# Kernel tuning notes

Measured on AMD Instinct MI355X. Metric: run time of the kernel, lower is better.

Reference implementation:

```python
import jax, jax.numpy as jnp
import numpy as np

B, T, C = 4, 2048, 768
H, D = 12, 64          # num_heads, head_size
R = 64                 # kv_lora_rank
ROPE_THETA = 10000.0


def setup_inputs() -> dict:
    key = jax.random.key(0)
    ks = jax.random.split(key, 8)
    s = lambda fan_in: 1.0 / np.sqrt(fan_in)
    return {
        "x":      jax.random.normal(ks[0], (B, T, C), jnp.float32),
        "Wq":     jax.random.normal(ks[1], (C, H * D), jnp.float32) * s(C),
        "Wdown":  jax.random.normal(ks[2], (C, R), jnp.float32) * s(C),
        "ln_g":   jnp.ones((R,), jnp.float32),
        "ln_b":   jnp.zeros((R,), jnp.float32),
        "Wup":    jax.random.normal(ks[3], (R, 2 * H * D), jnp.float32) * s(R),
        "Wo":     jax.random.normal(ks[4], (H * D, C), jnp.float32) * s(H * D),
        "bo":     jnp.zeros((C,), jnp.float32),
    }


def _rope_cos_sin(t, d, dtype):
    # freqs over half-dim, repeated twice (rotate-half convention)
    inv_freq = 1.0 / (ROPE_THETA ** (jnp.arange(0, d, 2, dtype=jnp.float32) / d))
    ang = jnp.arange(t, dtype=jnp.float32)[:, None] * inv_freq[None, :]  # [T, D/2]
    ang = jnp.concatenate([ang, ang], axis=-1)                            # [T, D]
    return jnp.cos(ang).astype(dtype), jnp.sin(ang).astype(dtype)


def _apply_rope(q, cos, sin):
    # q: [B, H, T, D]; cos/sin: [T, D]
    d2 = q.shape[-1] // 2
    rot = jnp.concatenate([-q[..., d2:], q[..., :d2]], axis=-1)
    return q * cos + rot * sin


def reference(x, Wq, Wdown, ln_g, ln_b, Wup, Wo, bo):
    b, t, c = x.shape
    q = (x @ Wq).reshape(b, t, H, D).transpose(0, 2, 1, 3)  # [B,H,T,D]

    ckv = x @ Wdown                                         # [B,T,R]
    mu = jnp.mean(ckv, axis=-1, keepdims=True)
    var = jnp.var(ckv, axis=-1, keepdims=True)
    ckv = (ckv - mu) * jax.lax.rsqrt(var + 1e-5) * ln_g + ln_b

    kv = (ckv @ Wup).reshape(b, t, 2, H, D)
    k = kv[:, :, 0].transpose(0, 2, 1, 3)                   # [B,H,T,D]
    v = kv[:, :, 1].transpose(0, 2, 1, 3)

    cos, sin = _rope_cos_sin(t, D, x.dtype)
    q = _apply_rope(q, cos, sin)
    k = _apply_rope(k, cos, sin)

    wei = jnp.einsum("bhqd,bhkd->bhqk", q, k) * (D ** -0.5)
    causal = jnp.tril(jnp.ones((t, t), bool))
    wei = jnp.where(causal, wei, -jnp.inf)
    wei = jax.nn.softmax(wei, axis=-1)                      # dropout: eval mode (identity)

    out = jnp.einsum("bhqk,bhkd->bhqd", wei, v)             # [B,H,T,D]
    out = out.transpose(0, 2, 1, 3).reshape(b, t, H * D)
    return out @ Wo + bo
```

## Files before the change

### kernel.cpp

```cpp
#include <hip/hip_runtime.h>
#include <hip/hip_bf16.h>
#include <math.h>

#define B_ 4
#define T_ 2048
#define C_ 768
#define H_ 12
#define D_ 64
#define R_ 64
#define BT_ (B_*T_)
#define HD_ (H_*D_)

typedef __attribute__((ext_vector_type(8))) short bf16x8;
typedef __attribute__((ext_vector_type(4))) float f32x4;
typedef __attribute__((ext_vector_type(16))) float f32x16;

__device__ inline short f2bf(float f) {
  union { float f; unsigned u; } x; x.f = f;
  unsigned r = x.u + 0x7fffu + ((x.u >> 16) & 1u);
  return (short)(r >> 16);
}
__device__ inline unsigned pk_bf16(float a, float b) {
#if __has_builtin(__builtin_amdgcn_cvt_pk_bf16_f32)
  auto t = __builtin_amdgcn_cvt_pk_bf16_f32(a, b);
  unsigned u; __builtin_memcpy(&u, &t, sizeof(unsigned)); return u;
#else
  union { float f; unsigned u; } x, y; x.f = a; y.f = b;
  unsigned ra = (x.u + 0x7fffu + ((x.u >> 16) & 1u)) >> 16;
  unsigned rb = (y.u + 0x7fffu + ((y.u >> 16) & 1u)) & 0xffff0000u;
  return ra | rb;
#endif
}
__device__ inline float fexp2(float x) {
#if __has_builtin(__builtin_amdgcn_exp2f)
  return __builtin_amdgcn_exp2f(x);
#else
  return exp2f(x);
#endif
}
__device__ inline void pswap(unsigned &a, unsigned &b) {
#if __has_builtin(__builtin_amdgcn_permlane32_swap)
  auto r = __builtin_amdgcn_permlane32_swap((int)a, (int)b, false, false);
  unsigned u[2]; __builtin_memcpy(u, &r, 8);
  a = u[0]; b = u[1];
#else
  unsigned ax = __shfl_xor(a, 32), bx = __shfl_xor(b, 32);
  bool hi = (threadIdx.x & 32) != 0;
  unsigned na = hi ? bx : a;
  unsigned nb = hi ? b : ax;
  a = na; b = nb;
#endif
}
typedef __attribute__((address_space(3))) unsigned lds_u32;
typedef __attribute__((address_space(1))) const unsigned glb_u32;
__device__ inline void gload_lds16(const void* g, void* l) {
  __builtin_amdgcn_global_load_lds((glb_u32*)g, (lds_u32*)l, 16, 0, 0);
}

__device__ inline void ttile(const float* __restrict__ src, short* __restrict__ dst,
                             int K, int N, int k0, int n0, int tid, float (*tl)[33]) {
  int tx = tid & 31, ty = tid >> 5;
  #pragma unroll
  for (int r = 0; r < 4; ++r)
    tl[ty + 8 * r][tx] = src[(size_t)(k0 + ty + 8 * r) * N + n0 + tx];
  __syncthreads();
  #pragma unroll
  for (int r = 0; r < 4; ++r)
    dst[(size_t)(n0 + ty + 8 * r) * K + k0 + tx] = f2bf(tl[tx][ty + 8 * r]);
}

__global__ __launch_bounds__(256) void prep_conv(
    const float* __restrict__ Wq, const float* __restrict__ Wd,
    const float* __restrict__ Wup, const float* __restrict__ Wo,
    short* __restrict__ W1T, short* __restrict__ WupT, short* __restrict__ WoT,
    float* __restrict__ cs, float* __restrict__ sn) {
  __shared__ float tl[32][33];
  int tid = threadIdx.x;
  int blk = blockIdx.x;
  if (blk < 576) {
    int tk = blk % 24, tn = blk / 24;
    ttile(Wq, W1T, 768, 768, tk * 32, tn * 32, tid, tl);
  } else if (blk < 624) {
    int l = blk - 576; int tk = l % 24, tn = l / 24;
    ttile(Wd, W1T + (size_t)768 * 768, 768, 64, tk * 32, tn * 32, tid, tl);
  } else if (blk < 720) {
    int l = blk - 624; int tk = l % 2, tn = l / 2;
    ttile(Wup, WupT, 64, 1536, tk * 32, tn * 32, tid, tl);
  } else if (blk < 1296) {
    int l = blk - 720; int tk = l % 24, tn = l / 24;
    ttile(Wo, WoT, 768, 768, tk * 32, tn * 32, tid, tl);
  } else {
    int base = (blk - 1296) * 1024;
    #pragma unroll
    for (int i = 0; i < 4; ++i) {
      int idx = base + tid + i * 256;
      int j = idx & 31, t = idx >> 5;
      float invf = exp2f(-(float)j * (13.287712379549449f / 32.f));
      float a = (float)t * invf;
      cs[idx] = cosf(a);
      sn[idx] = sinf(a);
    }
  }
}

#define SC2_ 0.18033688f

template<int MODE>
__global__ __launch_bounds__(256) void gemm128(
    const float* __restrict__ Af, const short* __restrict__ Ab,
    const short* __restrict__ Bt,
    int M, int N, int K,
    const float* __restrict__ bias, const float* __restrict__ bias2,
    short* __restrict__ ob0, short* __restrict__ ob1,
    const float* __restrict__ cs, const float* __restrict__ sn)
{
  constexpr int NBUF = (MODE == 0) ? 2 : 1;
  __shared__ short SM[NBUF * 2 * 128 * 64];
  const int m0 = blockIdx.x * 128;
  const int n0 = blockIdx.y * 128;
  const int tid = threadIdx.x, lane = tid & 63, w = tid >> 6;
  const int wr = w >> 1, wc = w & 1;
  const int fr = lane & 15, fk = (lane >> 4) * 8;
  const int rstage = lane >> 3;
  const int cstage = (lane & 7) * 8;

  f32x4 acc[4][4] = {};

  auto As = [&](int buf) -> short* { return SM + buf * 16384; };
  auto Bs = [&](int buf) -> short* { return SM + buf * 16384 + 8192; };

  auto compute = [&](const short* Asb, const short* Bsb) {
    #pragma unroll
    for (int kk = 0; kk < 64; kk += 32) {
      bf16x8 a[4], b[4];
      #pragma unroll
      for (int mi = 0; mi < 4; ++mi)
        a[mi] = *(const bf16x8*)&Asb[(wr * 64 + mi * 16 + fr) * 64 + kk + fk];
      #pragma unroll
      for (int ni = 0; ni < 4; ++ni)
        b[ni] = *(const bf16x8*)&Bsb[(wc * 64 + ni * 16 + fr) * 64 + kk + fk];
      #pragma unroll
      for (int mi = 0; mi < 4; ++mi)
        #pragma unroll
        for (int ni = 0; ni < 4; ++ni)
          acc[mi][ni] = __builtin_amdgcn_mfma_f32_16x16x32_bf16(a[mi], b[ni], acc[mi][ni], 0, 0, 0);
    }
  };

  auto stageB = [&](short* Bsb, int k0) {
    #pragma unroll
    for (int i = 0; i < 4; ++i) {
      int c = w * 4 + i;
      int r = c * 8 + rstage;
      gload_lds16(&Bt[(size_t)(n0 + r) * K + k0 + cstage], Bsb + c * 512);
    }
  };

  if constexpr (MODE == 0) {
    float4 fa[8];
    auto loadA = [&](int k0) {
      #pragma unroll
      for (int i = 0; i < 4; ++i) {
        int idx = tid + 256 * i;
        int row = idx >> 3, c8 = idx & 7;
        const float* src = Af + (size_t)(m0 + row) * 768 + k0 + c8 * 8;
        fa[2 * i]     = *(const float4*)(src);
        fa[2 * i + 1] = *(const float4*)(src + 4);
      }
    };
    auto writeA = [&](short* Asb) {
      #pragma unroll
      for (int i = 0; i < 4; ++i) {
        int idx = tid + 256 * i;
        int row = idx >> 3, c8 = idx & 7;
        uint4 uu;
        uu.x = pk_bf16(fa[2 * i].x,     fa[2 * i].y);
        uu.y = pk_bf16(fa[2 * i].z,     fa[2 * i].w);
        uu.z = pk_bf16(fa[2 * i + 1].x, fa[2 * i + 1].y);
        uu.w = pk_bf16(fa[2 * i + 1].z, fa[2 * i + 1].w);
        *(uint4*)&Asb[row * 64 + c8 * 8] = uu;
      }
    };

    loadA(0);
    stageB(Bs(0), 0);
    writeA(As(0));
    __syncthreads();

    int buf = 0;
    for (int k0 = 0; k0 < K; k0 += 64) {
      bool nxt = (k0 + 64 < K);
      if (nxt) { loadA(k0 + 64); stageB(Bs(buf ^ 1), k0 + 64); }
      compute(As(buf), Bs(buf));
      if (nxt) writeA(As(buf ^ 1));
      __syncthreads();
      buf ^= 1;
    }
  } else {
    #pragma unroll
    for (int i = 0; i < 4; ++i) {
      int c = w * 4 + i;
      int r = c * 8 + rstage;
      gload_lds16(&Ab[(size_t)(m0 + r) * K + cstage], As(0) + c * 512);
      gload_lds16(&Bt[(size_t)(n0 + r) * K + cstage], Bs(0) + c * 512);
    }
    __syncthreads();
    compute(As(0), Bs(0));
  }

  const int er = (lane >> 4) * 4, ec = lane & 15;
  const int cb = n0 + wc * 64;

  if (cb < 768) {
    int h = cb >> 6;
    #pragma unroll
    for (int mi = 0; mi < 4; ++mi)
      #pragma unroll
      for (int r = 0; r < 4; ++r) {
        int row = m0 + wr * 64 + mi * 16 + er + r;
        int t = row & (T_ - 1), bb = row >> 11;
        short* dst = ob0 + (((size_t)(bb * H_ + h)) * T_ + t) * 64;
        #pragma unroll
        for (int ni = 0; ni < 2; ++ni) {
          int d = ni * 16 + ec;
          float c = cs[t * 32 + d], s = sn[t * 32 + d];
          if constexpr (MODE == 0) { c *= SC2_; s *= SC2_; }
          float x0 = acc[mi][ni][r], x1 = acc[mi][ni + 2][r];
          dst[d]      = f2bf(x0 * c - x1 * s);
          dst[d + 32] = f2bf(x1 * c + x0 * s);
        }
      }
  } else if constexpr (MODE == 0) {
    if (cb == 768) {
      #pragma unroll
      for (int mi = 0; mi < 4; ++mi)
        #pragma unroll
        for (int r = 0; r < 4; ++r) {
          float s = 0.f, s2 = 0.f;
          #pragma unroll
          for (int ni = 0; ni < 4; ++ni) { float v = acc[mi][ni][r]; s += v; s2 += v*v; }
          #pragma unroll
          for (int off = 1; off < 16; off <<= 1) {
            s  += __shfl_xor(s, off);
            s2 += __shfl_xor(s2, off);
          }
          float mu = s * (1.f/64.f);
          float var = s2 * (1.f/64.f) - mu * mu;
          float rstd = rsqrtf(var + 1e-5f);
          int row = m0 + wr * 64 + mi * 16 + er + r;
          #pragma unroll
          for (int ni = 0; ni < 4; ++ni) {
            int d = ni * 16 + ec;
            ob1[(size_t)row * 64 + d] = f2bf((acc[mi][ni][r] - mu) * rstd * bias[d] + bias2[d]);
          }
        }
    }
  } else {
    __syncthreads();
    short* Wl = SM + w * 2560;
    int h = (cb - 768) >> 6;
    int bb = m0 >> 11;
    int dl = lane >> 2, tl = (lane & 3) * 8;
    #pragma unroll
    for (int hp = 0; hp < 2; ++hp) {
      #pragma unroll
      for (int mi2 = 0; mi2 < 2; ++mi2) {
        int mi = hp * 2 + mi2;
        int tl0 = mi2 * 16 + er;
        #pragma unroll
        for (int ni = 0; ni < 4; ++ni) {
          int d = ni * 16 + ec;
          uint2 uu;
          uu.x = pk_bf16(acc[mi][ni][0], acc[mi][ni][1]);
          uu.y = pk_bf16(acc[mi][ni][2], acc[mi][ni][3]);
          *(uint2*)&Wl[d * 40 + tl0] = uu;
        }
      }
      int tg0 = (m0 & (T_ - 1)) + wr * 64 + hp * 32;
      #pragma unroll
      for (int j = 0; j < 4; ++j) {
        int d = j * 16 + dl;
        uint4 vv = *(const uint4*)&Wl[d * 40 + tl];
        *(uint4*)&ob1[((size_t)(bb * H_ + h) * 64 + d) * T_ + tg0 + tl] = vv;
      }
    }
  }
}

__global__ __launch_bounds__(256) void gemm_out(
    const short* __restrict__ A, const short* __restrict__ Bt,
    int M, int N, int K,
    float* __restrict__ out0, const float* __restrict__ bias)
{
  __shared__ short SM[2 * (128 * 64 + 64 * 64)];
  const int m0 = blockIdx.x * 128;
  const int n0 = blockIdx.y * 64;
  const int tid = threadIdx.x, lane = tid & 63, w = tid >> 6;
  const int fr = lane & 15, fk = (lane >> 4) * 8;
  const int rstage = lane >> 3;
  const int cstage = (lane & 7) * 8;

  f32x4 acc[2][4] = {};

  auto As = [&](int buf) -> short* { return SM + buf * 12288; };
  auto Bs = [&](int buf) -> short* { return SM + buf * 12288 + 8192; };

  auto stage = [&](int buf, int k0) {
    #pragma unroll
    for (int i = 0; i < 4; ++i) {
      int c = w * 4 + i;
      int r = c * 8 + rstage;
      gload_lds16(&A[(size_t)(m0 + r) * K + k0 + cstage], As(buf) + c * 512);
    }
    #pragma unroll
    for (int i = 0; i < 2; ++i) {
      int c = w * 2 + i;
      int r = c * 8 + rstage;
      gload_lds16(&Bt[(size_t)(n0 + r) * K + k0 + cstage], Bs(buf) + c * 512);
    }
  };

  stage(0, 0);
  __syncthreads();

  int buf = 0;
  for (int k0 = 0; k0 < K; k0 += 64) {
    if (k0 + 64 < K) stage(buf ^ 1, k0 + 64);
    #pragma unroll
    for (int kk = 0; kk < 64; kk += 32) {
      bf16x8 a[2], b[4];
      a[0] = *(const bf16x8*)&As(buf)[(w * 32 +      fr) * 64 + kk + fk];
      a[1] = *(const bf16x8*)&As(buf)[(w * 32 + 16 + fr) * 64 + kk + fk];
      #pragma unroll
      for (int ni = 0; ni < 4; ++ni)
        b[ni] = *(const bf16x8*)&Bs(buf)[(ni * 16 + fr) * 64 + kk + fk];
      #pragma unroll
      for (int mi = 0; mi < 2; ++mi)
        #pragma unroll
        for (int ni = 0; ni < 4; ++ni)
          acc[mi][ni] = __builtin_amdgcn_mfma_f32_16x16x32_bf16(a[mi], b[ni], acc[mi][ni], 0, 0, 0);
    }
    __syncthreads();
    buf ^= 1;
  }

  const int er = (lane >> 4) * 4, ec = lane & 15;
  #pragma unroll
  for (int mi = 0; mi < 2; ++mi)
    #pragma unroll
    for (int r = 0; r < 4; ++r) {
      int row = m0 + w * 32 + mi * 16 + er + r;
      #pragma unroll
      for (int ni = 0; ni < 4; ++ni) {
        int col = n0 + ni * 16 + ec;
        out0[(size_t)row * N + col] = acc[mi][ni][r] + bias[col];
      }
    }
}

__global__ __launch_bounds__(256) void attn_mfma(
    const short* __restrict__ qgl, const short* __restrict__ kg,
    const short* __restrict__ vtg, short* __restrict__ o)
{
  __shared__ short SMa[2][2][8 * 512];

  const int bh = blockIdx.x;
  const int u  = 15 - blockIdx.y;
  const int tid = threadIdx.x, lane = tid & 63, w = tid >> 6;
  const int q32 = lane & 31, half = lane >> 5;
  const short* kb  = kg  + (size_t)bh * T_ * 64;
  const short* vtb = vtg + (size_t)bh * 64 * T_;
  const int b = bh / H_, h = bh - b * H_;

  const int wq = 4 * u + w;
  const int q0 = wq * 32;
  const int last_w = (wq >> 1) * 64;
  const int qidx = q0 + q32;
  const int kend = (2 * u + 1) * 64;

  const short* qrow = qgl + ((size_t)bh * T_ + qidx) * 64;
  bf16x8 bq[4];
  #pragma unroll
  for (int ks = 0; ks < 4; ++ks)
    bq[ks] = *(const bf16x8*)&qrow[ks * 16 + half * 8];

  f32x16 oacc[2] = {};
  float lrun = 0.f;

  auto stage = [&](int buf, int kt) {
    #pragma unroll
    for (int i = 0; i < 2; ++i) {
      int c = w * 2 + i;
      int kh = c >> 2, ks = c & 3;
      gload_lds16(kb + (size_t)(kt + kh * 32 + q32) * 64 + ks * 16 + half * 8,
                  &SMa[buf][0][c * 512]);
      gload_lds16(vtb + (size_t)(kh * 32 + q32) * T_ + kt + ks * 16 + half * 8,
                  &SMa[buf][1][c * 512]);
    }
  };

  stage(0, 0);
  __syncthreads();

  int cur = 0;
  for (int kt = 0; kt <= kend; kt += 64) {
    if (kt + 64 <= kend) stage(cur ^ 1, kt + 64);

    if (kt <= last_w) {
      const short* Kc = &SMa[cur][0][0];
      const short* Vc = &SMa[cur][1][0];
      const bool diag = (kt == last_w);
      const int dkh = diag ? (wq & 1) : 2;
      const bool skip1 = diag && ((wq & 1) == 0);

      bf16x8 bp[4];
      #pragma unroll
      for (int kh = 0; kh < 2; ++kh) {
        if (kh == 1 && skip1) break;
        f32x16 sacc = {};
        __builtin_amdgcn_s_setprio(1);
        #pragma unroll
        for (int ks = 0; ks < 4; ++ks) {
          bf16x8 a = *(const bf16x8*)&Kc[(kh * 4 + ks) * 512 + lane * 8];
          sacc = __builtin_amdgcn_mfma_f32_32x32x16_bf16(a, bq[ks], sacc, 0, 0, 0);
        }
        __builtin_amdgcn_s_setprio(0);
        float pv[16];
        if (kh != dkh) {
          #pragma unroll
          for (int r = 0; r < 16; ++r) pv[r] = fexp2(sacc[r]);
        } else {
          #pragma unroll
          for (int r = 0; r < 16; ++r) {
            int key = kt + kh * 32 + (r & 3) + 8 * (r >> 2) + 4 * half;
            pv[r] = (key <= qidx) ? fexp2(sacc[r]) : 0.f;
          }
        }
        float t0 = (pv[0] + pv[1]) + (pv[2] + pv[3]);
        float t1 = (pv[4] + pv[5]) + (pv[6] + pv[7]);
        float t2 = (pv[8] + pv[9]) + (pv[10] + pv[11]);
        float t3 = (pv[12] + pv[13]) + (pv[14] + pv[15]);
        lrun += (t0 + t1) + (t2 + t3);
        unsigned l0 = pk_bf16(pv[0],  pv[1]),  h0 = pk_bf16(pv[2],  pv[3]);
        unsigned l1 = pk_bf16(pv[4],  pv[5]),  h1 = pk_bf16(pv[6],  pv[7]);
        unsigned l2 = pk_bf16(pv[8],  pv[9]),  h2 = pk_bf16(pv[10], pv[11]);
        unsigned l3 = pk_bf16(pv[12], pv[13]), h3 = pk_bf16(pv[14], pv[15]);
        pswap(l0, l1); pswap(h0, h1);
        pswap(l2, l3); pswap(h2, h3);
        union { unsigned u[4]; bf16x8 v; } f0, f1;
        f0.u[0] = l0; f0.u[1] = h0; f0.u[2] = l1; f0.u[3] = h1;
        f1.u[0] = l2; f1.u[1] = h2; f1.u[2] = l3; f1.u[3] = h3;
        bp[2 * kh + 0] = f0.v;
        bp[2 * kh + 1] = f1.v;
      }

      __builtin_amdgcn_s_setprio(1);
      #pragma unroll
      for (int ks = 0; ks < 2; ++ks)
        #pragma unroll
        for (int dt = 0; dt < 2; ++dt) {
          bf16x8 av = *(const bf16x8*)&Vc[(dt * 4 + ks) * 512 + lane * 8];
          oacc[dt] = __builtin_amdgcn_mfma_f32_32x32x16_bf16(av, bp[ks], oacc[dt], 0, 0, 0);
        }
      if (!skip1) {
        #pragma unroll
        for (int ks = 2; ks < 4; ++ks)
          #pragma unroll
          for (int dt = 0; dt < 2; ++dt) {
            bf16x8 av = *(const bf16x8*)&Vc[(dt * 4 + ks) * 512 + lane * 8];
            oacc[dt] = __builtin_amdgcn_mfma_f32_32x32x16_bf16(av, bp[ks], oacc[dt], 0, 0, 0);
          }
      }
      __builtin_amdgcn_s_setprio(0);
    }

    __syncthreads();
    cur ^= 1;
  }

  float ltot = lrun + __shfl_xor(lrun, 32);
  float inv = 1.f / ltot;
  short* Pw = &SMa[0][0][0] + w * 2304;
  #pragma unroll
  for (int dt = 0; dt < 2; ++dt)
    #pragma unroll
    for (int g2 = 0; g2 < 4; ++g2) {
      uint2 uu;
      uu.x = pk_bf16(oacc[dt][4 * g2 + 0] * inv, oacc[dt][4 * g2 + 1] * inv);
      uu.y = pk_bf16(oacc[dt][4 * g2 + 2] * inv, oacc[dt][4 * g2 + 3] * inv);
      *(uint2*)&Pw[q32 * 72 + dt * 32 + 8 * g2 + 4 * half] = uu;
    }
  int row = lane >> 1, seg = lane & 1;
  int t = q0 + row;
  short* orow = o + ((size_t)(b * T_ + t)) * HD_ + h * 64 + seg * 32;
  #pragma unroll
  for (int i = 0; i < 4; ++i) {
    uint4 vv = *(const uint4*)&Pw[row * 72 + seg * 32 + i * 8];
    *(uint4*)&orow[i * 8] = vv;
  }
}

extern "C" void kernel_launch(void* const* d_in, const int* in_sizes, int n_in,
                              void* d_out, int out_size, void* d_ws, size_t ws_size,
                              hipStream_t stream) {
  (void)in_sizes; (void)n_in; (void)out_size; (void)ws_size;
  const float* x     = (const float*)d_in[0];
  const float* Wq    = (const float*)d_in[1];
  const float* Wdown = (const float*)d_in[2];
  const float* ln_g  = (const float*)d_in[3];
  const float* ln_b  = (const float*)d_in[4];
  const float* Wup   = (const float*)d_in[5];
  const float* Wo    = (const float*)d_in[6];
  const float* bo    = (const float*)d_in[7];
  float* out = (float*)d_out;

  char* w = (char*)d_ws;
  short* W1T    = (short*)w;  w += (size_t)896 * C_    * 2;
  short* WupT   = (short*)w;  w += (size_t)2*HD_ * R_  * 2;
  short* WoT    = (short*)w;  w += (size_t)HD_ * C_    * 2;
  short* ckv    = (short*)w;  w += (size_t)BT_ * R_    * 2;
  short* qb     = (short*)w;  w += (size_t)BT_ * HD_   * 2;
  short* kb     = (short*)w;  w += (size_t)BT_ * HD_   * 2;
  short* vt     = (short*)w;  w += (size_t)BT_ * HD_   * 2;
  short* att    = (short*)w;  w += (size_t)BT_ * HD_   * 2;
  float* cs_t   = (float*)w;  w += (size_t)T_ * 32 * 4;
  float* sn_t   = (float*)w;  w += (size_t)T_ * 32 * 4;

  prep_conv<<<1360, 256, 0, stream>>>(Wq, Wdown, Wup, Wo,
                                      W1T, WupT, WoT, cs_t, sn_t);

  gemm128<0><<<dim3(BT_/128, 7), 256, 0, stream>>>(
      x, nullptr, W1T, BT_, 832, C_, ln_g, ln_b, qb, ckv, cs_t, sn_t);

  gemm128<1><<<dim3(BT_/128, 12), 256, 0, stream>>>(
      nullptr, ckv, WupT, BT_, 2*HD_, R_, nullptr, nullptr, kb, vt, cs_t, sn_t);

  attn_mfma<<<dim3(B_*H_, 16), 256, 0, stream>>>(qb, kb, vt, att);

  gemm_out<<<dim3(BT_/128, 12), 256, 0, stream>>>(
      att, WoT, BT_, C_, HD_, out, bo);
}
```

Before: 194.4 us.

## Fuse all stages into one persistent cooperative kernel with grid syncs

Turns the five separate kernels into device bodies and runs them inside a single cooperative persistent kernel of 512 blocks, with grid.sync between stages. Attention tiles are handed out through an atomic work counter so blocks pick up the heavy causal tiles first. The aim is to remove launch gaps and tail idle time between stages. In exchange, every stage now uses a fixed 64KB shared allocation at two blocks per CU, which can lower occupancy and add grid-barrier cost. If the cooperative launch fails, it falls back to the separate kernels.

```diff
diff --git a/kernel.cpp b/kernel.cpp
--- a/kernel.cpp
+++ b/kernel.cpp
@@ -1,5 +1,6 @@
 #include <hip/hip_runtime.h>
 #include <hip/hip_bf16.h>
+#include <hip/hip_cooperative_groups.h>
 #include <math.h>
 
 #define B_ 4
@@ -57,8 +58,12 @@
   __builtin_amdgcn_global_load_lds((glb_u32*)g, (lds_u32*)l, 16, 0, 0);
 }
 
-__device__ inline void ttile(const float* __restrict__ src, short* __restrict__ dst,
-                             int K, int N, int k0, int n0, int tid, float (*tl)[33]) {
+#define SC2_ 0.18033688f
+
+
+__device__ __attribute__((always_inline)) inline void ttile(
+    const float* __restrict__ src, short* __restrict__ dst,
+    int K, int N, int k0, int n0, int tid, float (*tl)[33]) {
   int tx = tid & 31, ty = tid >> 5;
   #pragma unroll
   for (int r = 0; r < 4; ++r)
@@ -69,14 +74,11 @@
     dst[(size_t)(n0 + ty + 8 * r) * K + k0 + tx] = f2bf(tl[tx][ty + 8 * r]);
 }
 
-__global__ __launch_bounds__(256) void prep_conv(
-    const float* __restrict__ Wq, const float* __restrict__ Wd,
-    const float* __restrict__ Wup, const float* __restrict__ Wo,
-    short* __restrict__ W1T, short* __restrict__ WupT, short* __restrict__ WoT,
-    float* __restrict__ cs, float* __restrict__ sn) {
-  __shared__ float tl[32][33];
-  int tid = threadIdx.x;
-  int blk = blockIdx.x;
+__device__ __attribute__((always_inline)) inline void prep_unit(
+    int blk, int tid, char* smemc,
+    const float* Wq, const float* Wd, const float* Wup, const float* Wo,
+    short* W1T, short* WupT, short* WoT, float* cs, float* sn) {
+  float (*tl)[33] = (float(*)[33])smemc;
   if (blk < 576) {
     int tk = blk % 24, tn = blk / 24;
     ttile(Wq, W1T, 768, 768, tk * 32, tn * 32, tid, tl);
@@ -103,21 +105,16 @@
   }
 }
 
-#define SC2_ 0.18033688f
-
 template<int MODE>
-__global__ __launch_bounds__(256) void gemm128(
+__device__ __attribute__((always_inline)) inline void gemm128_body(
+    int m0, int n0, char* smemc,
     const float* __restrict__ Af, const short* __restrict__ Ab,
-    const short* __restrict__ Bt,
-    int M, int N, int K,
+    const short* __restrict__ Bt, int K,
     const float* __restrict__ bias, const float* __restrict__ bias2,
     short* __restrict__ ob0, short* __restrict__ ob1,
     const float* __restrict__ cs, const float* __restrict__ sn)
 {
-  constexpr int NBUF = (MODE == 0) ? 2 : 1;
-  __shared__ short SM[NBUF * 2 * 128 * 64];
-  const int m0 = blockIdx.x * 128;
-  const int n0 = blockIdx.y * 128;
+  short* SM = (short*)smemc;
   const int tid = threadIdx.x, lane = tid & 63, w = tid >> 6;
   const int wr = w >> 1, wc = w & 1;
   const int fr = lane & 15, fk = (lane >> 4) * 8;
@@ -287,14 +284,13 @@
   }
 }
 
-__global__ __launch_bounds__(256) void gemm_out(
+__device__ __attribute__((always_inline)) inline void gemmout_body(
+    int m0, int n0, char* smemc,
     const short* __restrict__ A, const short* __restrict__ Bt,
-    int M, int N, int K,
     float* __restrict__ out0, const float* __restrict__ bias)
 {
-  __shared__ short SM[2 * (128 * 64 + 64 * 64)];
-  const int m0 = blockIdx.x * 128;
-  const int n0 = blockIdx.y * 64;
+  short* SM = (short*)smemc;
+  const int K = HD_, N = C_;
   const int tid = threadIdx.x, lane = tid & 63, w = tid >> 6;
   const int fr = lane & 15, fk = (lane >> 4) * 8;
   const int rstage = lane >> 3;
@@ -358,14 +354,14 @@
     }
 }
 
-__global__ __launch_bounds__(256) void attn_mfma(
+__device__ __attribute__((always_inline)) inline void attn_body(
+    int bh, int u, char* smemc,
     const short* __restrict__ qgl, const short* __restrict__ kg,
     const short* __restrict__ vtg, short* __restrict__ o)
 {
-  __shared__ short SMa[2][2][8 * 512];
-
-  const int bh = blockIdx.x;
-  const int u  = 15 - blockIdx.y;
+  typedef short KVBUF[2][8 * 512];
+  KVBUF* SMa = (KVBUF*)smemc;
+
   const int tid = threadIdx.x, lane = tid & 63, w = tid >> 6;
   const int q32 = lane & 31, half = lane >> 5;
   const short* kb  = kg  + (size_t)bh * T_ * 64;
@@ -480,7 +476,7 @@
 
   float ltot = lrun + __shfl_xor(lrun, 32);
   float inv = 1.f / ltot;
-  short* Pw = &SMa[0][0][0] + w * 2304;
+  short* Pw = (short*)smemc + w * 2304;
   #pragma unroll
   for (int dt = 0; dt < 2; ++dt)
     #pragma unroll
@@ -498,6 +494,94 @@
     uint4 vv = *(const uint4*)&Pw[row * 72 + seg * 32 + i * 8];
     *(uint4*)&orow[i * 8] = vv;
   }
+}
+
+struct MegaArgs {
+  const float *x, *Wq, *Wd, *ln_g, *ln_b, *Wup, *Wo, *bo;
+  float *out;
+  short *W1T, *WupT, *WoT, *ckv, *qb, *kb, *vt, *att;
+  float *cs, *sn;
+  unsigned *qcnt;
+};
+
+namespace cg = cooperative_groups;
+
+__global__ __launch_bounds__(256, 2) void mega(MegaArgs A) {
+  __shared__ __align__(16) char SMEM[65536];
+  const int blk = blockIdx.x;
+  const int tid = threadIdx.x;
+  cg::grid_group grid = cg::this_grid();
+
+  if (blk == 0 && tid == 0) *A.qcnt = 0u;
+
+  for (int p = blk; p < 1360; p += 512) {
+    prep_unit(p, tid, SMEM, A.Wq, A.Wd, A.Wup, A.Wo, A.W1T, A.WupT, A.WoT, A.cs, A.sn);
+    __syncthreads();
+  }
+  grid.sync();
+
+  if (blk < 448) {
+    int bx = blk & 63, by = blk >> 6;
+    gemm128_body<0>(bx * 128, by * 128, SMEM, A.x, nullptr, A.W1T, 768,
+                    A.ln_g, A.ln_b, A.qb, A.ckv, A.cs, A.sn);
+  }
+  grid.sync();
+
+  for (int p = blk; p < 768; p += 512) {
+    int bx = p & 63, by = p >> 6;
+    gemm128_body<1>(bx * 128, by * 128, SMEM, nullptr, A.ckv, A.WupT, 64,
+                    nullptr, nullptr, A.kb, A.vt, A.cs, A.sn);
+    __syncthreads();
+  }
+  grid.sync();
+
+  unsigned* qslot = (unsigned*)(SMEM + 65532);
+  for (;;) {
+    __syncthreads();
+    if (tid == 0) *qslot = atomicAdd(A.qcnt, 1u);
+    __syncthreads();
+    unsigned q = *qslot;
+    if (q >= 768u) break;
+    attn_body((int)(q % 48u), 15 - (int)(q / 48u), SMEM, A.qb, A.kb, A.vt, A.att);
+  }
+  grid.sync();
+
+  for (int p = blk; p < 768; p += 512) {
+    int bx = p & 63, by = p >> 6;
+    gemmout_body(bx * 128, by * 64, SMEM, A.att, A.WoT, A.out, A.bo);
+    __syncthreads();
+  }
+}
+
+__global__ __launch_bounds__(256) void prep_conv_k(
+    const float* Wq, const float* Wd, const float* Wup, const float* Wo,
+    short* W1T, short* WupT, short* WoT, float* cs, float* sn) {
+  __shared__ __align__(16) char s[4352];
+  prep_unit(blockIdx.x, threadIdx.x, s, Wq, Wd, Wup, Wo, W1T, WupT, WoT, cs, sn);
+}
+__global__ __launch_bounds__(256) void gemm0_k(
+    const float* x, const short* W1T, const float* ln_g, const float* ln_b,
+    short* qb, short* ckv, const float* cs, const float* sn) {
+  __shared__ __align__(16) char s[65536];
+  gemm128_body<0>(blockIdx.x * 128, blockIdx.y * 128, s, x, nullptr, W1T, 768,
+                  ln_g, ln_b, qb, ckv, cs, sn);
+}
+__global__ __launch_bounds__(256) void gemm1_k(
+    const short* ckv, const short* WupT, short* kb, short* vt,
+    const float* cs, const float* sn) {
+  __shared__ __align__(16) char s[32768];
+  gemm128_body<1>(blockIdx.x * 128, blockIdx.y * 128, s, nullptr, ckv, WupT, 64,
+                  nullptr, nullptr, kb, vt, cs, sn);
+}
+__global__ __launch_bounds__(256) void attn_k(
+    const short* qb, const short* kb, const short* vt, short* att) {
+  __shared__ __align__(16) char s[32768];
+  attn_body(blockIdx.x, 15 - (int)blockIdx.y, s, qb, kb, vt, att);
+}
+__global__ __launch_bounds__(256) void gemmout_k(
+    const short* att, const short* WoT, float* out, const float* bo) {
+  __shared__ __align__(16) char s[49152];
+  gemmout_body(blockIdx.x * 128, blockIdx.y * 64, s, att, WoT, out, bo);
 }
 
 extern "C" void kernel_launch(void* const* d_in, const int* in_sizes, int n_in,
@@ -525,18 +609,23 @@
   short* att    = (short*)w;  w += (size_t)BT_ * HD_   * 2;
   float* cs_t   = (float*)w;  w += (size_t)T_ * 32 * 4;
   float* sn_t   = (float*)w;  w += (size_t)T_ * 32 * 4;
-
-  prep_conv<<<1360, 256, 0, stream>>>(Wq, Wdown, Wup, Wo,
-                                      W1T, WupT, WoT, cs_t, sn_t);
-
-  gemm128<0><<<dim3(BT_/128, 7), 256, 0, stream>>>(
-      x, nullptr, W1T, BT_, 832, C_, ln_g, ln_b, qb, ckv, cs_t, sn_t);
-
-  gemm128<1><<<dim3(BT_/128, 12), 256, 0, stream>>>(
-      nullptr, ckv, WupT, BT_, 2*HD_, R_, nullptr, nullptr, kb, vt, cs_t, sn_t);
-
-  attn_mfma<<<dim3(B_*H_, 16), 256, 0, stream>>>(qb, kb, vt, att);
-
-  gemm_out<<<dim3(BT_/128, 12), 256, 0, stream>>>(
-      att, WoT, BT_, C_, HD_, out, bo);
-}
+  unsigned* qcnt = (unsigned*)w; w += 64;
+
+  MegaArgs ma;
+  ma.x = x; ma.Wq = Wq; ma.Wd = Wdown; ma.ln_g = ln_g; ma.ln_b = ln_b;
+  ma.Wup = Wup; ma.Wo = Wo; ma.bo = bo; ma.out = out;
+  ma.W1T = W1T; ma.WupT = WupT; ma.WoT = WoT; ma.ckv = ckv;
+  ma.qb = qb; ma.kb = kb; ma.vt = vt; ma.att = att;
+  ma.cs = cs_t; ma.sn = sn_t; ma.qcnt = qcnt;
+  void* kargs[] = { &ma };
+
+  hipError_t e = hipLaunchCooperativeKernel((const void*)mega, dim3(512), dim3(256),
+                                            kargs, 0, stream);
+  if (e != hipSuccess) {
+    prep_conv_k<<<1360, 256, 0, stream>>>(Wq, Wdown, Wup, Wo, W1T, WupT, WoT, cs_t, sn_t);
+    gemm0_k<<<dim3(64, 7), 256, 0, stream>>>(x, W1T, ln_g, ln_b, qb, ckv, cs_t, sn_t);
+    gemm1_k<<<dim3(64, 12), 256, 0, stream>>>(ckv, WupT, kb, vt, cs_t, sn_t);
+    attn_k<<<dim3(48, 16), 256, 0, stream>>>(qb, kb, vt, att);
+    gemmout_k<<<dim3(64, 12), 256, 0, stream>>>(att, WoT, out, bo);
+  }
+}
```

Measured after the change: 474.5 us. +144.0%, slower.

## Absorb V up-projection into output weights and attend over shared latent

Applied to the files above, without the earlier changes.

Precomputes per-head products of the V half of Wup with Wo in the prep kernel. Attention then consumes the transposed normalized latent (shared across heads) instead of per-head V. gemm0 writes the latent in transposed layout, and the KV up-projection now only computes K. This removes the V half of the up-projection GEMM and its per-head V writes and reads, at the cost of a small fp32 weight-product in prep and extra bf16 rounding of the fused weight.

```diff
diff --git a/kernel.cpp b/kernel.cpp
--- a/kernel.cpp
+++ b/kernel.cpp
@@ -57,75 +57,96 @@
   __builtin_amdgcn_global_load_lds((glb_u32*)g, (lds_u32*)l, 16, 0, 0);
 }
 
-__device__ inline void ttile(const float* __restrict__ src, short* __restrict__ dst,
-                             int K, int N, int k0, int n0, int tid, float (*tl)[33]) {
+#define SC2_ 0.18033688f
+
+__device__ __attribute__((always_inline)) inline void ttile(
+    const float* __restrict__ src, short* __restrict__ dst,
+    int Kd, int Ns, int k0, int n0, int tid, float (*tl)[33]) {
   int tx = tid & 31, ty = tid >> 5;
   #pragma unroll
   for (int r = 0; r < 4; ++r)
-    tl[ty + 8 * r][tx] = src[(size_t)(k0 + ty + 8 * r) * N + n0 + tx];
+    tl[ty + 8 * r][tx] = src[(size_t)(k0 + ty + 8 * r) * Ns + n0 + tx];
   __syncthreads();
   #pragma unroll
   for (int r = 0; r < 4; ++r)
-    dst[(size_t)(n0 + ty + 8 * r) * K + k0 + tx] = f2bf(tl[tx][ty + 8 * r]);
+    dst[(size_t)(n0 + ty + 8 * r) * Kd + k0 + tx] = f2bf(tl[tx][ty + 8 * r]);
 }
 
 __global__ __launch_bounds__(256) void prep_conv(
     const float* __restrict__ Wq, const float* __restrict__ Wd,
     const float* __restrict__ Wup, const float* __restrict__ Wo,
-    short* __restrict__ W1T, short* __restrict__ WupT, short* __restrict__ WoT,
+    short* __restrict__ W1T, short* __restrict__ WupT, short* __restrict__ WvoT,
     float* __restrict__ cs, float* __restrict__ sn) {
-  __shared__ float tl[32][33];
-  int tid = threadIdx.x;
-  int blk = blockIdx.x;
+  __shared__ float SH[32 * 65 + 64 * 33];
+  float (*tl)[33] = (float(*)[33])SH;
+  int tid = threadIdx.x, blk = blockIdx.x;
   if (blk < 576) {
     int tk = blk % 24, tn = blk / 24;
     ttile(Wq, W1T, 768, 768, tk * 32, tn * 32, tid, tl);
   } else if (blk < 624) {
     int l = blk - 576; int tk = l % 24, tn = l / 24;
     ttile(Wd, W1T + (size_t)768 * 768, 768, 64, tk * 32, tn * 32, tid, tl);
-  } else if (blk < 720) {
+  } else if (blk < 672) {
     int l = blk - 624; int tk = l % 2, tn = l / 2;
     ttile(Wup, WupT, 64, 1536, tk * 32, tn * 32, tid, tl);
-  } else if (blk < 1296) {
-    int l = blk - 720; int tk = l % 24, tn = l / 24;
-    ttile(Wo, WoT, 768, 768, tk * 32, tn * 32, tid, tl);
+  } else if (blk < 1248) {
+    int l = blk - 672;
+    int h = l / 48, rem = l % 48, tc = rem >> 1, tr = rem & 1;
+    float* a  = SH;
+    float* bm = SH + 32 * 65;
+    #pragma unroll
+    for (int i = 0; i < 8; ++i) {
+      int idx = tid + i * 256;
+      int r = idx >> 6, d = idx & 63;
+      a[r * 65 + d] = Wup[(size_t)(tr * 32 + r) * 1536 + 768 + h * 64 + d];
+      int dd = idx >> 5, c = idx & 31;
+      bm[dd * 33 + c] = Wo[(size_t)(h * 64 + dd) * 768 + tc * 32 + c];
+    }
+    __syncthreads();
+    int r = tid & 31, cj = tid >> 5;
+    float s0 = 0.f, s1 = 0.f, s2 = 0.f, s3 = 0.f;
+    #pragma unroll
+    for (int d = 0; d < 64; ++d) {
+      float av = a[r * 65 + d];
+      const float* bp = &bm[d * 33 + cj * 4];
+      s0 += av * bp[0]; s1 += av * bp[1]; s2 += av * bp[2]; s3 += av * bp[3];
+    }
+    int colb = tc * 32 + cj * 4;
+    size_t krow = (size_t)(h * 64 + tr * 32 + r);
+    WvoT[(size_t)(colb + 0) * 768 + krow] = f2bf(s0);
+    WvoT[(size_t)(colb + 1) * 768 + krow] = f2bf(s1);
+    WvoT[(size_t)(colb + 2) * 768 + krow] = f2bf(s2);
+    WvoT[(size_t)(colb + 3) * 768 + krow] = f2bf(s3);
   } else {
-    int base = (blk - 1296) * 1024;
+    int base = (blk - 1248) * 1024;
     #pragma unroll
     for (int i = 0; i < 4; ++i) {
       int idx = base + tid + i * 256;
       int j = idx & 31, t = idx >> 5;
       float invf = exp2f(-(float)j * (13.287712379549449f / 32.f));
-      float a = (float)t * invf;
-      cs[idx] = cosf(a);
-      sn[idx] = sinf(a);
-    }
-  }
-}
-
-#define SC2_ 0.18033688f
-
-template<int MODE>
-__global__ __launch_bounds__(256) void gemm128(
-    const float* __restrict__ Af, const short* __restrict__ Ab,
-    const short* __restrict__ Bt,
-    int M, int N, int K,
+      float ang = (float)t * invf;
+      cs[idx] = cosf(ang);
+      sn[idx] = sinf(ang);
+    }
+  }
+}
+
+__global__ __launch_bounds__(256) void gemm0_k(
+    const float* __restrict__ Af, const short* __restrict__ Bt,
     const float* __restrict__ bias, const float* __restrict__ bias2,
-    short* __restrict__ ob0, short* __restrict__ ob1,
+    short* __restrict__ ob0, short* __restrict__ ob1, short* __restrict__ obT,
     const float* __restrict__ cs, const float* __restrict__ sn)
 {
-  constexpr int NBUF = (MODE == 0) ? 2 : 1;
-  __shared__ short SM[NBUF * 2 * 128 * 64];
+  constexpr int K = 768;
+  __shared__ short SM[2 * 16384];
   const int m0 = blockIdx.x * 128;
   const int n0 = blockIdx.y * 128;
   const int tid = threadIdx.x, lane = tid & 63, w = tid >> 6;
   const int wr = w >> 1, wc = w & 1;
   const int fr = lane & 15, fk = (lane >> 4) * 8;
-  const int rstage = lane >> 3;
-  const int cstage = (lane & 7) * 8;
+  const int rstage = lane >> 3, cstage = (lane & 7) * 8;
 
   f32x4 acc[4][4] = {};
-
   auto As = [&](int buf) -> short* { return SM + buf * 16384; };
   auto Bs = [&](int buf) -> short* { return SM + buf * 16384 + 8192; };
 
@@ -146,7 +167,6 @@
           acc[mi][ni] = __builtin_amdgcn_mfma_f32_16x16x32_bf16(a[mi], b[ni], acc[mi][ni], 0, 0, 0);
     }
   };
-
   auto stageB = [&](short* Bsb, int k0) {
     #pragma unroll
     for (int i = 0; i < 4; ++i) {
@@ -156,56 +176,44 @@
     }
   };
 
-  if constexpr (MODE == 0) {
-    float4 fa[8];
-    auto loadA = [&](int k0) {
-      #pragma unroll
-      for (int i = 0; i < 4; ++i) {
-        int idx = tid + 256 * i;
-        int row = idx >> 3, c8 = idx & 7;
-        const float* src = Af + (size_t)(m0 + row) * 768 + k0 + c8 * 8;
-        fa[2 * i]     = *(const float4*)(src);
-        fa[2 * i + 1] = *(const float4*)(src + 4);
-      }
-    };
-    auto writeA = [&](short* Asb) {
-      #pragma unroll
-      for (int i = 0; i < 4; ++i) {
-        int idx = tid + 256 * i;
-        int row = idx >> 3, c8 = idx & 7;
-        uint4 uu;
-        uu.x = pk_bf16(fa[2 * i].x,     fa[2 * i].y);
-        uu.y = pk_bf16(fa[2 * i].z,     fa[2 * i].w);
-        uu.z = pk_bf16(fa[2 * i + 1].x, fa[2 * i + 1].y);
-        uu.w = pk_bf16(fa[2 * i + 1].z, fa[2 * i + 1].w);
-        *(uint4*)&Asb[row * 64 + c8 * 8] = uu;
-      }
-    };
-
-    loadA(0);
-    stageB(Bs(0), 0);
-    writeA(As(0));
+  float4 fa[8];
+  auto loadA = [&](int k0) {
+    #pragma unroll
+    for (int i = 0; i < 4; ++i) {
+      int idx = tid + 256 * i;
+      int row = idx >> 3, c8 = idx & 7;
+      const float* src = Af + (size_t)(m0 + row) * 768 + k0 + c8 * 8;
+      fa[2 * i]     = *(const float4*)(src);
+      fa[2 * i + 1] = *(const float4*)(src + 4);
+    }
+  };
+  auto writeA = [&](short* Asb) {
+    #pragma unroll
+    for (int i = 0; i < 4; ++i) {
+      int idx = tid + 256 * i;
+      int row = idx >> 3, c8 = idx & 7;
+      uint4 uu;
+      uu.x = pk_bf16(fa[2 * i].x,     fa[2 * i].y);
+      uu.y = pk_bf16(fa[2 * i].z,     fa[2 * i].w);
+      uu.z = pk_bf16(fa[2 * i + 1].x, fa[2 * i + 1].y);
+      uu.w = pk_bf16(fa[2 * i + 1].z, fa[2 * i + 1].w);
+      *(uint4*)&Asb[row * 64 + c8 * 8] = uu;
+    }
+  };
+
+  loadA(0);
+  stageB(Bs(0), 0);
+  writeA(As(0));
+  __syncthreads();
+
+  int buf = 0;
+  for (int k0 = 0; k0 < K; k0 += 64) {
+    bool nxt = (k0 + 64 < K);
+    if (nxt) { loadA(k0 + 64); stageB(Bs(buf ^ 1), k0 + 64); }
+    compute(As(buf), Bs(buf));
+    if (nxt) writeA(As(buf ^ 1));
     __syncthreads();
-
-    int buf = 0;
-    for (int k0 = 0; k0 < K; k0 += 64) {
-      bool nxt = (k0 + 64 < K);
-      if (nxt) { loadA(k0 + 64); stageB(Bs(buf ^ 1), k0 + 64); }
-      compute(As(buf), Bs(buf));
-      if (nxt) writeA(As(buf ^ 1));
-      __syncthreads();
-      buf ^= 1;
-    }
-  } else {
-    #pragma unroll
-    for (int i = 0; i < 4; ++i) {
-      int c = w * 4 + i;
-      int r = c * 8 + rstage;
-      gload_lds16(&Ab[(size_t)(m0 + r) * K + cstage], As(0) + c * 512);
-      gload_lds16(&Bt[(size_t)(n0 + r) * K + cstage], Bs(0) + c * 512);
-    }
-    __syncthreads();
-    compute(As(0), Bs(0));
+    buf ^= 1;
   }
 
   const int er = (lane >> 4) * 4, ec = lane & 15;
@@ -223,56 +231,51 @@
         #pragma unroll
         for (int ni = 0; ni < 2; ++ni) {
           int d = ni * 16 + ec;
-          float c = cs[t * 32 + d], s = sn[t * 32 + d];
-          if constexpr (MODE == 0) { c *= SC2_; s *= SC2_; }
+          float c = cs[t * 32 + d] * SC2_, s = sn[t * 32 + d] * SC2_;
           float x0 = acc[mi][ni][r], x1 = acc[mi][ni + 2][r];
           dst[d]      = f2bf(x0 * c - x1 * s);
           dst[d + 32] = f2bf(x1 * c + x0 * s);
         }
       }
-  } else if constexpr (MODE == 0) {
-    if (cb == 768) {
-      #pragma unroll
-      for (int mi = 0; mi < 4; ++mi)
+  } else if (cb == 768) {
+    short* Wl = SM + w * 2560;
+    int bb = m0 >> 11;
+    int dl = lane >> 2, tlo = (lane & 3) * 8;
+    #pragma unroll
+    for (int hp = 0; hp < 2; ++hp) {
+      #pragma unroll
+      for (int mi2 = 0; mi2 < 2; ++mi2) {
+        int mi = hp * 2 + mi2;
+        short vb[4][4];
         #pragma unroll
         for (int r = 0; r < 4; ++r) {
           float s = 0.f, s2 = 0.f;
           #pragma unroll
-          for (int ni = 0; ni < 4; ++ni) { float v = acc[mi][ni][r]; s += v; s2 += v*v; }
+          for (int ni = 0; ni < 4; ++ni) { float v = acc[mi][ni][r]; s += v; s2 += v * v; }
           #pragma unroll
           for (int off = 1; off < 16; off <<= 1) {
             s  += __shfl_xor(s, off);
             s2 += __shfl_xor(s2, off);
           }
-          float mu = s * (1.f/64.f);
-          float var = s2 * (1.f/64.f) - mu * mu;
+          float mu = s * (1.f / 64.f);
+          float var = s2 * (1.f / 64.f) - mu * mu;
           float rstd = rsqrtf(var + 1e-5f);
           int row = m0 + wr * 64 + mi * 16 + er + r;
           #pragma unroll
           for (int ni = 0; ni < 4; ++ni) {
             int d = ni * 16 + ec;
-            ob1[(size_t)row * 64 + d] = f2bf((acc[mi][ni][r] - mu) * rstd * bias[d] + bias2[d]);
+            short q = f2bf((acc[mi][ni][r] - mu) * rstd * bias[d] + bias2[d]);
+            vb[r][ni] = q;
+            ob1[(size_t)row * 64 + d] = q;
           }
         }
-    }
-  } else {
-    __syncthreads();
-    short* Wl = SM + w * 2560;
-    int h = (cb - 768) >> 6;
-    int bb = m0 >> 11;
-    int dl = lane >> 2, tl = (lane & 3) * 8;
-    #pragma unroll
-    for (int hp = 0; hp < 2; ++hp) {
-      #pragma unroll
-      for (int mi2 = 0; mi2 < 2; ++mi2) {
-        int mi = hp * 2 + mi2;
         int tl0 = mi2 * 16 + er;
         #pragma unroll
         for (int ni = 0; ni < 4; ++ni) {
           int d = ni * 16 + ec;
           uint2 uu;
-          uu.x = pk_bf16(acc[mi][ni][0], acc[mi][ni][1]);
-          uu.y = pk_bf16(acc[mi][ni][2], acc[mi][ni][3]);
+          uu.x = (unsigned)(unsigned short)vb[0][ni] | ((unsigned)(unsigned short)vb[1][ni] << 16);
+          uu.y = (unsigned)(unsigned short)vb[2][ni] | ((unsigned)(unsigned short)vb[3][ni] << 16);
           *(uint2*)&Wl[d * 40 + tl0] = uu;
         }
       }
@@ -280,80 +283,72 @@
       #pragma unroll
       for (int j = 0; j < 4; ++j) {
         int d = j * 16 + dl;
-        uint4 vv = *(const uint4*)&Wl[d * 40 + tl];
-        *(uint4*)&ob1[((size_t)(bb * H_ + h) * 64 + d) * T_ + tg0 + tl] = vv;
+        uint4 vv = *(const uint4*)&Wl[d * 40 + tlo];
+        *(uint4*)&obT[((size_t)(bb * 64 + d)) * T_ + tg0 + tlo] = vv;
       }
     }
   }
 }
 
-__global__ __launch_bounds__(256) void gemm_out(
+__global__ __launch_bounds__(256) void gemm1_k(
     const short* __restrict__ A, const short* __restrict__ Bt,
-    int M, int N, int K,
-    float* __restrict__ out0, const float* __restrict__ bias)
+    short* __restrict__ ob0,
+    const float* __restrict__ cs, const float* __restrict__ sn)
 {
-  __shared__ short SM[2 * (128 * 64 + 64 * 64)];
+  constexpr int K = 64;
+  __shared__ short SM[2 * 8192];
+  short* As = SM;
+  short* Bs = SM + 8192;
   const int m0 = blockIdx.x * 128;
-  const int n0 = blockIdx.y * 64;
+  const int n0 = blockIdx.y * 128;
   const int tid = threadIdx.x, lane = tid & 63, w = tid >> 6;
+  const int wr = w >> 1, wc = w & 1;
   const int fr = lane & 15, fk = (lane >> 4) * 8;
-  const int rstage = lane >> 3;
-  const int cstage = (lane & 7) * 8;
-
-  f32x4 acc[2][4] = {};
-
-  auto As = [&](int buf) -> short* { return SM + buf * 12288; };
-  auto Bs = [&](int buf) -> short* { return SM + buf * 12288 + 8192; };
-
-  auto stage = [&](int buf, int k0) {
-    #pragma unroll
-    for (int i = 0; i < 4; ++i) {
-      int c = w * 4 + i;
-      int r = c * 8 + rstage;
-      gload_lds16(&A[(size_t)(m0 + r) * K + k0 + cstage], As(buf) + c * 512);
-    }
-    #pragma unroll
-    for (int i = 0; i < 2; ++i) {
-      int c = w * 2 + i;
-      int r = c * 8 + rstage;
-      gload_lds16(&Bt[(size_t)(n0 + r) * K + k0 + cstage], Bs(buf) + c * 512);
-    }
-  };
-
-  stage(0, 0);
+  const int rstage = lane >> 3, cstage = (lane & 7) * 8;
+
+  f32x4 acc[4][4] = {};
+
+  #pragma unroll
+  for (int i = 0; i < 4; ++i) {
+    int c = w * 4 + i;
+    int r = c * 8 + rstage;
+    gload_lds16(&A[(size_t)(m0 + r) * K + cstage], As + c * 512);
+    gload_lds16(&Bt[(size_t)(n0 + r) * K + cstage], Bs + c * 512);
+  }
   __syncthreads();
-
-  int buf = 0;
-  for (int k0 = 0; k0 < K; k0 += 64) {
-    if (k0 + 64 < K) stage(buf ^ 1, k0 + 64);
-    #pragma unroll
-    for (int kk = 0; kk < 64; kk += 32) {
-      bf16x8 a[2], b[4];
-      a[0] = *(const bf16x8*)&As(buf)[(w * 32 +      fr) * 64 + kk + fk];
-      a[1] = *(const bf16x8*)&As(buf)[(w * 32 + 16 + fr) * 64 + kk + fk];
+  #pragma unroll
+  for (int kk = 0; kk < 64; kk += 32) {
+    bf16x8 a[4], b[4];
+    #pragma unroll
+    for (int mi = 0; mi < 4; ++mi)
+      a[mi] = *(const bf16x8*)&As[(wr * 64 + mi * 16 + fr) * 64 + kk + fk];
+    #pragma unroll
+    for (int ni = 0; ni < 4; ++ni)
+      b[ni] = *(const bf16x8*)&Bs[(wc * 64 + ni * 16 + fr) * 64 + kk + fk];
+    #pragma unroll
+    for (int mi = 0; mi < 4; ++mi)
       #pragma unroll
       for (int ni = 0; ni < 4; ++ni)
-        b[ni] = *(const bf16x8*)&Bs(buf)[(ni * 16 + fr) * 64 + kk + fk];
-      #pragma unroll
-      for (int mi = 0; mi < 2; ++mi)
-        #pragma unroll
-        for (int ni = 0; ni < 4; ++ni)
-          acc[mi][ni] = __builtin_amdgcn_mfma_f32_16x16x32_bf16(a[mi], b[ni], acc[mi][ni], 0, 0, 0);
-    }
-    __syncthreads();
-    buf ^= 1;
+        acc[mi][ni] = __builtin_amdgcn_mfma_f32_16x16x32_bf16(a[mi], b[ni], acc[mi][ni], 0, 0, 0);
   }
 
   const int er = (lane >> 4) * 4, ec = lane & 15;
-  #pragma unroll
-  for (int mi = 0; mi < 2; ++mi)
+  const int cb = n0 + wc * 64;
+  int h = cb >> 6;
+  #pragma unroll
+  for (int mi = 0; mi < 4; ++mi)
     #pragma unroll
     for (int r = 0; r < 4; ++r) {
-      int row = m0 + w * 32 + mi * 16 + er + r;
-      #pragma unroll
-      for (int ni = 0; ni < 4; ++ni) {
-        int col = n0 + ni * 16 + ec;
-        out0[(size_t)row * N + col] = acc[mi][ni][r] + bias[col];
+      int row = m0 + wr * 64 + mi * 16 + er + r;
+      int t = row & (T_ - 1), bb = row >> 11;
+      short* dst = ob0 + (((size_t)(bb * H_ + h)) * T_ + t) * 64;
+      #pragma unroll
+      for (int ni = 0; ni < 2; ++ni) {
+        int d = ni * 16 + ec;
+        float c = cs[t * 32 + d], s = sn[t * 32 + d];
+        float x0 = acc[mi][ni][r], x1 = acc[mi][ni + 2][r];
+        dst[d]      = f2bf(x0 * c - x1 * s);
+        dst[d + 32] = f2bf(x1 * c + x0 * s);
       }
     }
 }
@@ -368,9 +363,9 @@
   const int u  = 15 - blockIdx.y;
   const int tid = threadIdx.x, lane = tid & 63, w = tid >> 6;
   const int q32 = lane & 31, half = lane >> 5;
+  const int b = bh / H_, h = bh - b * H_;
   const short* kb  = kg  + (size_t)bh * T_ * 64;
-  const short* vtb = vtg + (size_t)bh * 64 * T_;
-  const int b = bh / H_, h = bh - b * H_;
+  const short* vtb = vtg + (size_t)b * 64 * T_;
 
   const int wq = 4 * u + w;
   const int q0 = wq * 32;
@@ -500,6 +495,76 @@
   }
 }
 
+__global__ __launch_bounds__(256) void gemm_out(
+    const short* __restrict__ A, const short* __restrict__ Bt,
+    float* __restrict__ out0, const float* __restrict__ bias)
+{
+  constexpr int K = HD_, N = C_;
+  __shared__ short SM[2 * (8192 + 4096)];
+  const int m0 = blockIdx.x * 128;
+  const int n0 = blockIdx.y * 64;
+  const int tid = threadIdx.x, lane = tid & 63, w = tid >> 6;
+  const int fr = lane & 15, fk = (lane >> 4) * 8;
+  const int rstage = lane >> 3, cstage = (lane & 7) * 8;
+
+  f32x4 acc[2][4] = {};
+
+  auto As = [&](int buf) -> short* { return SM + buf * 12288; };
+  auto Bs = [&](int buf) -> short* { return SM + buf * 12288 + 8192; };
+
+  auto stage = [&](int buf, int k0) {
+    #pragma unroll
+    for (int i = 0; i < 4; ++i) {
+      int c = w * 4 + i;
+      int r = c * 8 + rstage;
+      gload_lds16(&A[(size_t)(m0 + r) * K + k0 + cstage], As(buf) + c * 512);
+    }
+    #pragma unroll
+    for (int i = 0; i < 2; ++i) {
+      int c = w * 2 + i;
+      int r = c * 8 + rstage;
+      gload_lds16(&Bt[(size_t)(n0 + r) * K + k0 + cstage], Bs(buf) + c * 512);
+    }
+  };
+
+  stage(0, 0);
+  __syncthreads();
+
+  int buf = 0;
+  for (int k0 = 0; k0 < K; k0 += 64) {
+    if (k0 + 64 < K) stage(buf ^ 1, k0 + 64);
+    #pragma unroll
+    for (int kk = 0; kk < 64; kk += 32) {
+      bf16x8 a[2], b[4];
+      a[0] = *(const bf16x8*)&As(buf)[(w * 32 +      fr) * 64 + kk + fk];
+      a[1] = *(const bf16x8*)&As(buf)[(w * 32 + 16 + fr) * 64 + kk + fk];
+      #pragma unroll
+      for (int ni = 0; ni < 4; ++ni)
+        b[ni] = *(const bf16x8*)&Bs(buf)[(ni * 16 + fr) * 64 + kk + fk];
+      #pragma unroll
+      for (int mi = 0; mi < 2; ++mi)
+        #pragma unroll
+        for (int ni = 0; ni < 4; ++ni)
+          acc[mi][ni] = __builtin_amdgcn_mfma_f32_16x16x32_bf16(a[mi], b[ni], acc[mi][ni], 0, 0, 0);
+    }
+    __syncthreads();
+    buf ^= 1;
+  }
+
+  const int er = (lane >> 4) * 4, ec = lane & 15;
+  #pragma unroll
+  for (int mi = 0; mi < 2; ++mi)
+    #pragma unroll
+    for (int r = 0; r < 4; ++r) {
+      int row = m0 + w * 32 + mi * 16 + er + r;
+      #pragma unroll
+      for (int ni = 0; ni < 4; ++ni) {
+        int col = n0 + ni * 16 + ec;
+        out0[(size_t)row * N + col] = acc[mi][ni][r] + bias[col];
+      }
+    }
+}
+
 extern "C" void kernel_launch(void* const* d_in, const int* in_sizes, int n_in,
                               void* d_out, int out_size, void* d_ws, size_t ws_size,
                               hipStream_t stream) {
@@ -516,27 +581,26 @@
 
   char* w = (char*)d_ws;
   short* W1T    = (short*)w;  w += (size_t)896 * C_    * 2;
-  short* WupT   = (short*)w;  w += (size_t)2*HD_ * R_  * 2;
-  short* WoT    = (short*)w;  w += (size_t)HD_ * C_    * 2;
+  short* WupT   = (short*)w;  w += (size_t)HD_ * R_    * 2;
+  short* WvoT   = (short*)w;  w += (size_t)C_ * HD_    * 2;
   short* ckv    = (short*)w;  w += (size_t)BT_ * R_    * 2;
+  short* ckvT   = (short*)w;  w += (size_t)B_ * R_ * T_ * 2;
   short* qb     = (short*)w;  w += (size_t)BT_ * HD_   * 2;
   short* kb     = (short*)w;  w += (size_t)BT_ * HD_   * 2;
-  short* vt     = (short*)w;  w += (size_t)BT_ * HD_   * 2;
   short* att    = (short*)w;  w += (size_t)BT_ * HD_   * 2;
   float* cs_t   = (float*)w;  w += (size_t)T_ * 32 * 4;
   float* sn_t   = (float*)w;  w += (size_t)T_ * 32 * 4;
 
-  prep_conv<<<1360, 256, 0, stream>>>(Wq, Wdown, Wup, Wo,
-                                      W1T, WupT, WoT, cs_t, sn_t);
-
-  gemm128<0><<<dim3(BT_/128, 7), 256, 0, stream>>>(
-      x, nullptr, W1T, BT_, 832, C_, ln_g, ln_b, qb, ckv, cs_t, sn_t);
-
-  gemm128<1><<<dim3(BT_/128, 12), 256, 0, stream>>>(
-      nullptr, ckv, WupT, BT_, 2*HD_, R_, nullptr, nullptr, kb, vt, cs_t, sn_t);
-
-  attn_mfma<<<dim3(B_*H_, 16), 256, 0, stream>>>(qb, kb, vt, att);
-
-  gemm_out<<<dim3(BT_/128, 12), 256, 0, stream>>>(
-      att, WoT, BT_, C_, HD_, out, bo);
-}
+  prep_conv<<<1312, 256, 0, stream>>>(Wq, Wdown, Wup, Wo,
+                                      W1T, WupT, WvoT, cs_t, sn_t);
+
+  gemm0_k<<<dim3(BT_/128, 7), 256, 0, stream>>>(
+      x, W1T, ln_g, ln_b, qb, ckv, ckvT, cs_t, sn_t);
+
+  gemm1_k<<<dim3(BT_/128, 6), 256, 0, stream>>>(
+      ckv, WupT, kb, cs_t, sn_t);
+
+  attn_mfma<<<dim3(B_*H_, 16), 256, 0, stream>>>(qb, kb, ckvT, att);
+
+  gemm_out<<<dim3(BT_/128, 12), 256, 0, stream>>>(att, WvoT, out, bo);
+}
```

Result: no change. 195.7 us (+0.6%).
